# Kernel optimization log

Measured on AMD Instinct MI355X. Metric: run time of the kernel, lower is better.

Reference implementation:

```python
import jax, jax.numpy as jnp
import numpy as np

T, B = 100, 256
NUM_IN, NUM_HID, NUM_OUT = 784, 512, 10
BETA = 0.95
THRESH = 1.0   # snntorch Leaky default threshold
SLOPE = 25.0   # surrogate.fast_sigmoid default slope

# Heaviside spike with fast_sigmoid surrogate gradient (snntorch semantics)
@jax.custom_vjp
def spike_fn(x):
    return (x > 0).astype(x.dtype)

def _spike_fwd(x):
    return spike_fn(x), x

def _spike_bwd(x, g):
    return (g / (SLOPE * jnp.abs(x) + 1.0) ** 2,)

spike_fn.defvjp(_spike_fwd, _spike_bwd)

def setup_inputs() -> dict:
    key = jax.random.key(0)
    ks = jax.random.split(key, 5)
    x = jax.random.normal(ks[0], (T, B, NUM_IN), dtype=jnp.float32)
    w1 = jax.random.normal(ks[1], (NUM_HID, NUM_IN), dtype=jnp.float32) / np.float32(np.sqrt(NUM_IN))
    b1 = jax.random.normal(ks[2], (NUM_HID,), dtype=jnp.float32) * 0.01
    w2 = jax.random.normal(ks[3], (NUM_OUT, NUM_HID), dtype=jnp.float32) / np.float32(np.sqrt(NUM_HID))
    b2 = jax.random.normal(ks[4], (NUM_OUT,), dtype=jnp.float32) * 0.01
    return {"x": x, "w1": w1, "b1": b1, "w2": w2, "b2": b2}

def _snn_forward(x, w1, b1, w2, b2):
    mem1_0 = jnp.zeros((B, NUM_HID), x.dtype)
    mem2_0 = jnp.zeros((B, NUM_OUT), x.dtype)

    def step(carry, xt):
        mem1, mem2 = carry
        # layer 1: Linear + Leaky (reset-by-subtraction, reset detached as in snntorch)
        cur1 = xt @ w1.T + b1
        reset1 = jax.lax.stop_gradient(spike_fn(mem1 - THRESH))
        mem1 = BETA * mem1 + cur1 - reset1 * THRESH
        spk1 = spike_fn(mem1 - THRESH)
        # layer 2
        cur2 = spk1 @ w2.T + b2
        reset2 = jax.lax.stop_gradient(spike_fn(mem2 - THRESH))
        mem2 = BETA * mem2 + cur2 - reset2 * THRESH
        spk2 = spike_fn(mem2 - THRESH)
        return (mem1, mem2), (cur2, spk2, spk1, mem2, mem1)

    _, ys = jax.lax.scan(step, (mem1_0, mem2_0), x)
    # ys = (cur_list, spk_list, spk_hidden_list, mem_list, mem_hidden_list), stacked over T
    return ys

def reference(x, w1, b1, w2, b2):
    return _snn_forward(x, w1, b1, w2, b2)
```

## Files before the change

kernel.cpp:

```cpp
#include <hip/hip_runtime.h>
#include <stdint.h>

#define T_STEPS 100
#define BATCH   256
#define NIN     784
#define NHID    512
#define NOUT    10


#define BM 128
#define BN 128
#define BK 8
#define PANEL_K 384

__global__ __launch_bounds__(256) void gemm1_dual(
    const float* __restrict__ X, const float* __restrict__ W,
    float* __restrict__ C1, float* __restrict__ C2)
{
    __shared__ float As[2][BK][BM + 4];
    __shared__ float Bs[2][BK][BN + 4];

    const int tid = threadIdx.x;
    const int bm  = blockIdx.x * BM;
    const int bn  = blockIdx.y * BN;
    const int kb  = blockIdx.z ? PANEL_K : 0;
    float* __restrict__ C = blockIdx.z ? C2 : C1;

    const int row  = tid >> 1;
    const int koff = (tid & 1) * 4;

    const int w    = tid >> 6;
    const int lane = tid & 63;
    const int tm   = (w & 1) * 64 + (lane & 7) * 8;
    const int tn   = (w >> 1) * 64 + (lane >> 3) * 8;

    float acc[8][8];
    #pragma unroll
    for (int i = 0; i < 8; ++i)
        #pragma unroll
        for (int j = 0; j < 8; ++j) acc[i][j] = 0.f;

    const float* Xp = X + (size_t)(bm + row) * NIN + kb + koff;
    const float* Wp = W + (size_t)(bn + row) * NIN + kb + koff;

    float4 pa = *(const float4*)(Xp);
    float4 pb = *(const float4*)(Wp);
    As[0][koff+0][row] = pa.x; As[0][koff+1][row] = pa.y;
    As[0][koff+2][row] = pa.z; As[0][koff+3][row] = pa.w;
    Bs[0][koff+0][row] = pb.x; Bs[0][koff+1][row] = pb.y;
    Bs[0][koff+2][row] = pb.z; Bs[0][koff+3][row] = pb.w;

    const int NITER = PANEL_K / BK;
    for (int it = 0; it < NITER; ++it) {
        const int cur = it & 1;
        __syncthreads();

        if (it + 1 < NITER) {
            const int k0 = (it + 1) * BK;
            pa = *(const float4*)(Xp + k0);
            pb = *(const float4*)(Wp + k0);
        }

        #pragma unroll
        for (int kk = 0; kk < BK; ++kk) {
            float4 av0 = *(const float4*)&As[cur][kk][tm];
            float4 av1 = *(const float4*)&As[cur][kk][tm + 4];
            float4 bv0 = *(const float4*)&Bs[cur][kk][tn];
            float4 bv1 = *(const float4*)&Bs[cur][kk][tn + 4];
            float a[8] = {av0.x, av0.y, av0.z, av0.w, av1.x, av1.y, av1.z, av1.w};
            float b[8] = {bv0.x, bv0.y, bv0.z, bv0.w, bv1.x, bv1.y, bv1.z, bv1.w};
            #pragma unroll
            for (int i = 0; i < 8; ++i)
                #pragma unroll
                for (int j = 0; j < 8; ++j)
                    acc[i][j] = fmaf(a[i], b[j], acc[i][j]);
        }

        if (it + 1 < NITER) {
            const int nxt = cur ^ 1;
            As[nxt][koff+0][row] = pa.x; As[nxt][koff+1][row] = pa.y;
            As[nxt][koff+2][row] = pa.z; As[nxt][koff+3][row] = pa.w;
            Bs[nxt][koff+0][row] = pb.x; Bs[nxt][koff+1][row] = pb.y;
            Bs[nxt][koff+2][row] = pb.z; Bs[nxt][koff+3][row] = pb.w;
        }
    }

    #pragma unroll
    for (int i = 0; i < 8; ++i) {
        size_t r = (size_t)(bm + tm + i) * NHID + bn + tn;
        *(float4*)&C[r]     = make_float4(acc[i][0], acc[i][1], acc[i][2], acc[i][3]);
        *(float4*)&C[r + 4] = make_float4(acc[i][4], acc[i][5], acc[i][6], acc[i][7]);
    }
}

__global__ __launch_bounds__(512) void leaky_hidden_fused(
    float* __restrict__ mem_io,
    const float* c2,
    float* spk_out,
    const float* __restrict__ X,
    const float* __restrict__ W1,
    const float* __restrict__ b1)
{
    __shared__ float4 xs4[T_STEPS][4];
    __shared__ float  p1s[2][8][256];
    __shared__ float  p2s[2][8][256];

    const int tid  = threadIdx.x;
    const int lane256 = tid & 255;
    const int base = blockIdx.x * 256;
    const size_t STRIDE = (size_t)BATCH * NHID;
    const int bb = base >> 9;
    const size_t col = (size_t)base + lane256;

    {
        const float* xbase = X + (size_t)bb * NIN + 768;
        for (int e = tid; e < T_STEPS * 4; e += 512) {
            const int t = e >> 2, q = e & 3;
            xs4[t][q] = *(const float4*)(xbase + (size_t)t * BATCH * NIN + q * 4);
        }
    }

    const bool producer = (tid >= 256);

    float wt[16];
    float bias = 0.f;
    float mem  = 0.f;

    if (producer) {
        float v1[8], v2[8];
        #pragma unroll
        for (int j = 0; j < 8; ++j) {
            v1[j] = mem_io[col + (size_t)j * STRIDE];
            v2[j] = c2[col + (size_t)j * STRIDE];
        }
        #pragma unroll
        for (int j = 0; j < 8; ++j) {
            p1s[0][j][lane256] = v1[j];
            p2s[0][j][lane256] = v2[j];
        }
    } else {
        const int h = (int)(col & (NHID - 1));
        const float* wp = W1 + (size_t)h * NIN + 768;
        float4 w0  = *(const float4*)(wp);
        float4 w1v = *(const float4*)(wp + 4);
        float4 w2v = *(const float4*)(wp + 8);
        float4 w3v = *(const float4*)(wp + 12);
        wt[0]=w0.x;  wt[1]=w0.y;  wt[2]=w0.z;  wt[3]=w0.w;
        wt[4]=w1v.x; wt[5]=w1v.y; wt[6]=w1v.z; wt[7]=w1v.w;
        wt[8]=w2v.x; wt[9]=w2v.y; wt[10]=w2v.z; wt[11]=w2v.w;
        wt[12]=w3v.x; wt[13]=w3v.y; wt[14]=w3v.z; wt[15]=w3v.w;
        bias = b1[h];
    }

    __syncthreads();

    for (int c = 0; c <= 12; ++c) {
        if (producer) {
            if (c < 12) {
                const int t0 = (c + 1) * 8;
                const int nb = (c + 1 == 12) ? 4 : 8;
                float v1[8], v2[8];
                #pragma unroll
                for (int j = 0; j < 8; ++j) {
                    if (j < nb) {
                        v1[j] = mem_io[col + (size_t)(t0 + j) * STRIDE];
                        v2[j] = c2[col + (size_t)(t0 + j) * STRIDE];
                    }
                }
                const int pb = (c + 1) & 1;
                #pragma unroll
                for (int j = 0; j < 8; ++j) {
                    if (j < nb) {
                        p1s[pb][j][lane256] = v1[j];
                        p2s[pb][j][lane256] = v2[j];
                    }
                }
            }
        } else {
            const int nt = (c == 12) ? 4 : 8;
            const int cb = c & 1;
            #pragma unroll
            for (int j = 0; j < 8; ++j) {
                if (j < nt) {
                    const int t = c * 8 + j;
                    const float p1 = p1s[cb][j][lane256];
                    const float p2 = p2s[cb][j][lane256];
                    float4 v0 = xs4[t][0], v1 = xs4[t][1];
                    float4 v2 = xs4[t][2], v3 = xs4[t][3];
                    float a = 0.f;
                    a = fmaf(v0.x, wt[0], a);  a = fmaf(v0.y, wt[1], a);
                    a = fmaf(v0.z, wt[2], a);  a = fmaf(v0.w, wt[3], a);
                    a = fmaf(v1.x, wt[4], a);  a = fmaf(v1.y, wt[5], a);
                    a = fmaf(v1.z, wt[6], a);  a = fmaf(v1.w, wt[7], a);
                    a = fmaf(v2.x, wt[8], a);  a = fmaf(v2.y, wt[9], a);
                    a = fmaf(v2.z, wt[10], a); a = fmaf(v2.w, wt[11], a);
                    a = fmaf(v3.x, wt[12], a); a = fmaf(v3.y, wt[13], a);
                    a = fmaf(v3.z, wt[14], a); a = fmaf(v3.w, wt[15], a);

                    const float cur = __fadd_rn(__fadd_rn(__fadd_rn(p1, p2), a), bias);
                    const float rst = (mem > 1.0f) ? 1.0f : 0.0f;
                    mem = __fsub_rn(__fadd_rn(__fmul_rn(0.95f, mem), cur), rst);

                    const size_t off = col + (size_t)t * STRIDE;
                    spk_out[off] = (mem > 1.0f) ? 1.0f : 0.0f;
                    mem_io[off]  = mem;
                }
            }
        }
        __syncthreads();
    }
}

#define G2_ROWS 32

__global__ __launch_bounds__(320) void gemm2_f64(
    const float* __restrict__ spk1, const float* __restrict__ W2,
    const float* __restrict__ b2, float* __restrict__ cur2)
{
    __shared__ float w2s[NOUT * NHID];
    const int tid = threadIdx.x;
    for (int i = tid; i < NOUT * NHID; i += 320) w2s[i] = W2[i];
    __syncthreads();

    const int r = tid / NOUT;
    const int o = tid % NOUT;
    const size_t m = (size_t)blockIdx.x * G2_ROWS + r;
    const float* rowp = spk1 + m * NHID;
    const float* wp   = w2s + o * NHID;
    double dot = 0.0;
    #pragma unroll 4
    for (int k = 0; k < NHID; k += 4) {
        float4 s  = *(const float4*)(rowp + k);
        float4 wv = *(const float4*)(wp + k);
        dot = fma((double)s.x, (double)wv.x, dot);
        dot = fma((double)s.y, (double)wv.y, dot);
        dot = fma((double)s.z, (double)wv.z, dot);
        dot = fma((double)s.w, (double)wv.w, dot);
    }
    cur2[m * NOUT + o] = (float)(dot + (double)b2[o]);
}

__global__ __launch_bounds__(256) void leaky_out_kernel(
    const float* __restrict__ cur2, float* __restrict__ spk2,
    float* __restrict__ mem2)
{
    const int idx = blockIdx.x * blockDim.x + threadIdx.x;
    if (idx >= BATCH * NOUT) return;
    const int STRIDE = BATCH * NOUT;

    float cur[T_STEPS];
    #pragma unroll
    for (int t = 0; t < T_STEPS; ++t)
        cur[t] = cur2[(size_t)t * STRIDE + idx];

    float mem = 0.f;
    #pragma unroll
    for (int t = 0; t < T_STEPS; ++t) {
        const float rst = (mem > 1.0f) ? 1.0f : 0.0f;
        mem = __fsub_rn(__fadd_rn(__fmul_rn(0.95f, mem), cur[t]), rst);
        const size_t off = (size_t)t * STRIDE + idx;
        spk2[off] = (mem > 1.0f) ? 1.0f : 0.0f;
        mem2[off] = mem;
    }
}

extern "C" void kernel_launch(void* const* d_in, const int* in_sizes, int n_in,
                              void* d_out, int out_size, void* d_ws, size_t ws_size,
                              hipStream_t stream) {
    const float* x  = (const float*)d_in[0];
    const float* w1 = (const float*)d_in[1];
    const float* b1 = (const float*)d_in[2];
    const float* w2 = (const float*)d_in[3];
    const float* b2 = (const float*)d_in[4];

    float* out = (float*)d_out;
    float* cur2_out = out;
    float* spk2_out = out + 256000;
    float* spk1_out = out + 512000;
    float* mem2_out = out + 13619200;
    float* mem1_out = out + 13875200;

    const int M = T_STEPS * BATCH;

    const size_t p2_bytes = (size_t)M * NHID * sizeof(float);
    float* p2buf = (d_ws != nullptr && ws_size >= p2_bytes)
                       ? (float*)d_ws : spk1_out;

    dim3 gp(M / BM, NHID / BN, 2);
    gemm1_dual<<<gp, 256, 0, stream>>>(x, w1, mem1_out, p2buf);

    leaky_hidden_fused<<<(BATCH * NHID) / 256, 512, 0, stream>>>(
        mem1_out, p2buf, spk1_out, x, w1, b1);

    gemm2_f64<<<M / G2_ROWS, 320, 0, stream>>>(spk1_out, w2, b2, cur2_out);

    leaky_out_kernel<<<(BATCH * NOUT + 255) / 256, 256, 0, stream>>>(
        cur2_out, spk2_out, mem2_out);
}
```

Before: 468.9 us.

## Enlarge GEMM1 M-tile to 256 rows and pad W2 shared rows

The first-layer GEMM tile grows from 128x128 to 256x128. Each thread now computes two 8x8 sub-tiles that share the same B fragment, and A loads are restructured so each thread stages one full row. This raises register use per thread and halves the number of blocks, which may hurt occupancy or wave fill on the GPU. Separately, the W2 staging buffer in gemm2 gets its rows padded by 4 floats to reduce LDS bank conflicts across output neurons.

```diff
diff --git a/kernel.cpp b/kernel.cpp
--- a/kernel.cpp
+++ b/kernel.cpp
@@ -8,7 +8,7 @@
 #define NOUT    10
 
 
-#define BM 128
+#define BM 256
 #define BN 128
 #define BK 8
 #define PANEL_K 384
@@ -26,29 +26,34 @@
     const int kb  = blockIdx.z ? PANEL_K : 0;
     float* __restrict__ C = blockIdx.z ? C2 : C1;
 
-    const int row  = tid >> 1;
-    const int koff = (tid & 1) * 4;
+    const int rowB  = tid >> 1;
+    const int koffB = (tid & 1) * 4;
 
     const int w    = tid >> 6;
     const int lane = tid & 63;
-    const int tm   = (w & 1) * 64 + (lane & 7) * 8;
+    const int tm   = (w & 1) * 128 + (lane & 7) * 8;
     const int tn   = (w >> 1) * 64 + (lane >> 3) * 8;
 
-    float acc[8][8];
+    float acc[2][8][8];
     #pragma unroll
-    for (int i = 0; i < 8; ++i)
-        #pragma unroll
-        for (int j = 0; j < 8; ++j) acc[i][j] = 0.f;
-
-    const float* Xp = X + (size_t)(bm + row) * NIN + kb + koff;
-    const float* Wp = W + (size_t)(bn + row) * NIN + kb + koff;
-
-    float4 pa = *(const float4*)(Xp);
-    float4 pb = *(const float4*)(Wp);
-    As[0][koff+0][row] = pa.x; As[0][koff+1][row] = pa.y;
-    As[0][koff+2][row] = pa.z; As[0][koff+3][row] = pa.w;
-    Bs[0][koff+0][row] = pb.x; Bs[0][koff+1][row] = pb.y;
-    Bs[0][koff+2][row] = pb.z; Bs[0][koff+3][row] = pb.w;
+    for (int h = 0; h < 2; ++h)
+        #pragma unroll
+        for (int i = 0; i < 8; ++i)
+            #pragma unroll
+            for (int j = 0; j < 8; ++j) acc[h][i][j] = 0.f;
+
+    const float* Xp = X + (size_t)(bm + tid) * NIN + kb;
+    const float* Wp = W + (size_t)(bn + rowB) * NIN + kb + koffB;
+
+    float4 pa0 = *(const float4*)(Xp);
+    float4 pa1 = *(const float4*)(Xp + 4);
+    float4 pb  = *(const float4*)(Wp);
+    As[0][0][tid] = pa0.x; As[0][1][tid] = pa0.y;
+    As[0][2][tid] = pa0.z; As[0][3][tid] = pa0.w;
+    As[0][4][tid] = pa1.x; As[0][5][tid] = pa1.y;
+    As[0][6][tid] = pa1.z; As[0][7][tid] = pa1.w;
+    Bs[0][koffB+0][rowB] = pb.x; Bs[0][koffB+1][rowB] = pb.y;
+    Bs[0][koffB+2][rowB] = pb.z; Bs[0][koffB+3][rowB] = pb.w;
 
     const int NITER = PANEL_K / BK;
     for (int it = 0; it < NITER; ++it) {
@@ -57,40 +62,52 @@
 
         if (it + 1 < NITER) {
             const int k0 = (it + 1) * BK;
-            pa = *(const float4*)(Xp + k0);
-            pb = *(const float4*)(Wp + k0);
+            pa0 = *(const float4*)(Xp + k0);
+            pa1 = *(const float4*)(Xp + k0 + 4);
+            pb  = *(const float4*)(Wp + k0);
         }
 
         #pragma unroll
         for (int kk = 0; kk < BK; ++kk) {
             float4 av0 = *(const float4*)&As[cur][kk][tm];
             float4 av1 = *(const float4*)&As[cur][kk][tm + 4];
+            float4 av2 = *(const float4*)&As[cur][kk][tm + 64];
+            float4 av3 = *(const float4*)&As[cur][kk][tm + 68];
             float4 bv0 = *(const float4*)&Bs[cur][kk][tn];
             float4 bv1 = *(const float4*)&Bs[cur][kk][tn + 4];
-            float a[8] = {av0.x, av0.y, av0.z, av0.w, av1.x, av1.y, av1.z, av1.w};
-            float b[8] = {bv0.x, bv0.y, bv0.z, bv0.w, bv1.x, bv1.y, bv1.z, bv1.w};
+            float a0[8] = {av0.x, av0.y, av0.z, av0.w, av1.x, av1.y, av1.z, av1.w};
+            float a1[8] = {av2.x, av2.y, av2.z, av2.w, av3.x, av3.y, av3.z, av3.w};
+            float b [8] = {bv0.x, bv0.y, bv0.z, bv0.w, bv1.x, bv1.y, bv1.z, bv1.w};
             #pragma unroll
             for (int i = 0; i < 8; ++i)
                 #pragma unroll
-                for (int j = 0; j < 8; ++j)
-                    acc[i][j] = fmaf(a[i], b[j], acc[i][j]);
+                for (int j = 0; j < 8; ++j) {
+                    acc[0][i][j] = fmaf(a0[i], b[j], acc[0][i][j]);
+                    acc[1][i][j] = fmaf(a1[i], b[j], acc[1][i][j]);
+                }
         }
 
         if (it + 1 < NITER) {
             const int nxt = cur ^ 1;
-            As[nxt][koff+0][row] = pa.x; As[nxt][koff+1][row] = pa.y;
-            As[nxt][koff+2][row] = pa.z; As[nxt][koff+3][row] = pa.w;
-            Bs[nxt][koff+0][row] = pb.x; Bs[nxt][koff+1][row] = pb.y;
-            Bs[nxt][koff+2][row] = pb.z; Bs[nxt][koff+3][row] = pb.w;
+            As[nxt][0][tid] = pa0.x; As[nxt][1][tid] = pa0.y;
+            As[nxt][2][tid] = pa0.z; As[nxt][3][tid] = pa0.w;
+            As[nxt][4][tid] = pa1.x; As[nxt][5][tid] = pa1.y;
+            As[nxt][6][tid] = pa1.z; As[nxt][7][tid] = pa1.w;
+            Bs[nxt][koffB+0][rowB] = pb.x; Bs[nxt][koffB+1][rowB] = pb.y;
+            Bs[nxt][koffB+2][rowB] = pb.z; Bs[nxt][koffB+3][rowB] = pb.w;
         }
     }
 
     #pragma unroll
-    for (int i = 0; i < 8; ++i) {
-        size_t r = (size_t)(bm + tm + i) * NHID + bn + tn;
-        *(float4*)&C[r]     = make_float4(acc[i][0], acc[i][1], acc[i][2], acc[i][3]);
-        *(float4*)&C[r + 4] = make_float4(acc[i][4], acc[i][5], acc[i][6], acc[i][7]);
-    }
+    for (int h = 0; h < 2; ++h)
+        #pragma unroll
+        for (int i = 0; i < 8; ++i) {
+            size_t r = (size_t)(bm + tm + h * 64 + i) * NHID + bn + tn;
+            *(float4*)&C[r]     = make_float4(acc[h][i][0], acc[h][i][1],
+                                              acc[h][i][2], acc[h][i][3]);
+            *(float4*)&C[r + 4] = make_float4(acc[h][i][4], acc[h][i][5],
+                                              acc[h][i][6], acc[h][i][7]);
+        }
 }
 
 __global__ __launch_bounds__(512) void leaky_hidden_fused(
@@ -212,21 +229,23 @@
 }
 
 #define G2_ROWS 32
+#define W2PAD  (NHID + 4)
 
 __global__ __launch_bounds__(320) void gemm2_f64(
     const float* __restrict__ spk1, const float* __restrict__ W2,
     const float* __restrict__ b2, float* __restrict__ cur2)
 {
-    __shared__ float w2s[NOUT * NHID];
+    __shared__ float w2s[NOUT][W2PAD];
     const int tid = threadIdx.x;
-    for (int i = tid; i < NOUT * NHID; i += 320) w2s[i] = W2[i];
+    for (int i = tid; i < NOUT * NHID; i += 320)
+        w2s[i >> 9][i & 511] = W2[i];
     __syncthreads();
 
     const int r = tid / NOUT;
     const int o = tid % NOUT;
     const size_t m = (size_t)blockIdx.x * G2_ROWS + r;
     const float* rowp = spk1 + m * NHID;
-    const float* wp   = w2s + o * NHID;
+    const float* wp   = &w2s[o][0];
     double dot = 0.0;
     #pragma unroll 4
     for (int k = 0; k < NHID; k += 4) {
```

New measurement: 639.3 us. 36.3% more time.
